# Kernel tuning notes

Measured on AMD Instinct MI355X. Metric: run time of the kernel, lower is better.

## Reference

```python
import jax, jax.numpy as jnp
import numpy as np

D = 2048          # input_dim == dec_hidden_size
S = 16384         # src_time_steps
H = 250           # projection hidden (hard-coded in module)


def setup_inputs() -> dict:
    key = jax.random.key(0)
    ks = jax.random.split(key, 12)
    sc_d = 1.0 / np.sqrt(D)
    sc_3d = 1.0 / np.sqrt(3 * D)
    sc_h = 1.0 / np.sqrt(H)
    return {
        "s_prev": jax.random.normal(ks[0], (1, 1, D), jnp.float32),
        "enc_hs": jax.random.normal(ks[1], (1, S, D), jnp.float32),
        "cur_men_rep": jax.random.normal(ks[2], (1, 1, D), jnp.float32),
        "src_mask": jax.random.randint(ks[3], (1, S), 0, 2, jnp.int32),
        "W_info": jax.random.normal(ks[4], (D, D), jnp.float32) * sc_d,
        "W_ctx": jax.random.normal(ks[5], (D, D), jnp.float32) * sc_d,
        "W_q": jax.random.normal(ks[6], (D, D), jnp.float32) * sc_d,
        "b_q": jnp.zeros((D,), jnp.float32),
        "W_p1": jax.random.normal(ks[7], (H, 3 * D), jnp.float32) * sc_3d,
        "b_p1": jnp.zeros((H,), jnp.float32),
        "W_p2": jax.random.normal(ks[8], (1, H), jnp.float32) * sc_h,
        "b_p2": jnp.zeros((1,), jnp.float32),
    }


def reference(s_prev, enc_hs, cur_men_rep, src_mask,
              W_info, W_ctx, W_q, b_q, W_p1, b_p1, W_p2, b_p2):
    # dh = linear_info(cur_men_rep): [1,1,D]; uh = linear_ctx(enc_hs): [1,S,D]
    dh = jnp.einsum('bqe,de->bqd', cur_men_rep, W_info)
    uh = jnp.einsum('bse,de->bsd', enc_hs, W_ctx)
    wq = jnp.einsum('bqe,de->bqd', s_prev, W_q) + b_q
    # cat(uh, wq.repeat, dh.repeat) -> tanh : [1,S,3D]
    wquh = jnp.tanh(jnp.concatenate(
        [uh, jnp.broadcast_to(wq, uh.shape), jnp.broadcast_to(dh, uh.shape)],
        axis=2))
    # projection: Linear(3D,250) -> Dropout(eval: identity) -> ReLU -> Linear(250,1)
    h = jax.nn.relu(jnp.einsum('bsk,hk->bsh', wquh, W_p1) + b_p1)
    scores = (jnp.einsum('bsh,oh->bso', h, W_p2) + b_p2).squeeze()   # [S] (B=1)
    scores = jnp.where(src_mask.squeeze().astype(bool), -jnp.inf, scores)
    attn = jax.nn.softmax(scores, axis=-1)                            # [S]
    ctx = jnp.sum(enc_hs * attn[None, :, None], axis=1)               # [1,D]
    return attn, ctx
```

## Files before the change

### kernel.cpp

```cpp
#include <hip/hip_runtime.h>
#include <hip/hip_bf16.h>
#include <stdint.h>

#define DD 2048
#define SS 16384
#define HH 250
#define GEMMB_GRID 264

typedef __attribute__((ext_vector_type(8))) short bf16x8;
typedef __attribute__((ext_vector_type(4))) float f32x4;

__device__ __forceinline__ unsigned short f2bf(float f){
  union { float f; uint32_t u; } v; v.f = f;
  uint32_t u = v.u;
  return (unsigned short)((u + 0x7fffu + ((u >> 16) & 1u)) >> 16);
}
__device__ __forceinline__ float fast_tanh(float x){
  return 1.0f - 2.0f / (1.0f + __expf(2.0f * x));
}
__device__ __forceinline__ void gl_lds16(const void* g, void* l){
  __builtin_amdgcn_global_load_lds((const __attribute__((address_space(1))) void*)g,
                                   (__attribute__((address_space(3))) void*)l, 16, 0, 0);
}

__global__ __launch_bounds__(256) void mega_kernel(
    const float* __restrict__ W_ctx, unsigned short* __restrict__ wctxb,
    const float* __restrict__ W_p1, unsigned short* __restrict__ wp1ab,
    const float* __restrict__ s_prev, const float* __restrict__ cmr,
    const float* __restrict__ Wq, const float* __restrict__ bq,
    const float* __restrict__ Winfo,
    float* __restrict__ twq, float* __restrict__ tdh,
    const int* __restrict__ mask, int* __restrict__ idx, int* __restrict__ cpos,
    int* __restrict__ mcount)
{
  const int b = blockIdx.x, t = threadIdx.x;
  if(b < 512){
    for(int i = b * 256 + t; i < (DD * DD) / 8; i += 512 * 256){
      const float4* p = (const float4*)(W_ctx + (size_t)i * 8);
      float4 a = p[0], c = p[1];
      bf16x8 v;
      v[0]=(short)f2bf(a.x); v[1]=(short)f2bf(a.y); v[2]=(short)f2bf(a.z); v[3]=(short)f2bf(a.w);
      v[4]=(short)f2bf(c.x); v[5]=(short)f2bf(c.y); v[6]=(short)f2bf(c.z); v[7]=(short)f2bf(c.w);
      *(bf16x8*)(wctxb + (size_t)i * 8) = v;
    }
  } else if(b < 768){
    int g = (b - 512) * 256 + t;
    int row = g >> 8, col = (g & 255) * 8;
    int rc = row < HH ? row : HH - 1;
    const float* s = W_p1 + (size_t)rc * (3 * DD) + col;
    bf16x8 v;
    #pragma unroll
    for(int j = 0; j < 8; j++) v[j] = (row < HH) ? (short)f2bf(s[j]) : (short)0;
    *(bf16x8*)(wp1ab + (size_t)g * 8) = v;
  } else if(b < 1792){
    int vb = b - 768;
    int wid = t >> 6, lane = t & 63;
    bool isq = vb < 512;
    int r = (isq ? vb : vb - 512) * 4 + wid;
    const float* M = (isq ? Wq : Winfo) + (size_t)r * DD;
    const float* x = isq ? s_prev : cmr;
    float s = 0.f;
    for(int i = lane; i < DD; i += 64) s += M[i] * x[i];
    #pragma unroll
    for(int o = 32; o; o >>= 1) s += __shfl_xor(s, o);
    if(lane == 0){
      if(isq) twq[r] = fast_tanh(s + bq[r]);
      else    tdh[r] = fast_tanh(s);
    }
  } else {
    __shared__ int cnt[256];
    const int base = t * 64;
    int c = 0;
    for(int i = 0; i < 64; i++) c += (mask[base + i] == 0);
    cnt[t] = c;
    __syncthreads();
    for(int off = 1; off < 256; off <<= 1){
      int v = (t >= off) ? cnt[t - off] : 0;
      __syncthreads();
      cnt[t] += v;
      __syncthreads();
    }
    int p = cnt[t] - c;
    for(int i = 0; i < 64; i++){
      int fi = base + i;
      if(mask[fi] == 0){ idx[p] = fi; cpos[fi] = p; p++; }
      else cpos[fi] = -1;
    }
    if(t == 255){
      int tot = cnt[255];
      mcount[0] = tot;
      mcount[1] = (tot + 255) & ~255;
      mcount[2] = (tot + 63) & ~63;
    }
  }
}

__global__ __launch_bounds__(256) void conv_enc_kernel(
    const float* __restrict__ enc, const int* __restrict__ idx,
    const int* __restrict__ mcount, unsigned short* __restrict__ out,
    const float* __restrict__ wp1, const float* __restrict__ bp1,
    const float* __restrict__ twq, const float* __restrict__ tdh,
    float* __restrict__ bias2)
{
  const int b = blockIdx.x, t = threadIdx.x;
  if(b < 2048){
    const int mc0 = mcount[0], mc1 = mcount[1];
    #pragma unroll
    for(int r = 0; r < 8; r++){
      int j = b * 8 + r;
      if(j >= mc1) return;
      unsigned short* o = out + (size_t)j * DD + t * 8;
      if(j >= mc0){
        bf16x8 z;
        #pragma unroll
        for(int i = 0; i < 8; i++) z[i] = 0;
        *(bf16x8*)o = z;
      } else {
        const float4* p = (const float4*)(enc + (size_t)idx[j] * DD + t * 8);
        float4 a = p[0], c = p[1];
        bf16x8 v;
        v[0]=(short)f2bf(a.x); v[1]=(short)f2bf(a.y); v[2]=(short)f2bf(a.z); v[3]=(short)f2bf(a.w);
        v[4]=(short)f2bf(c.x); v[5]=(short)f2bf(c.y); v[6]=(short)f2bf(c.z); v[7]=(short)f2bf(c.w);
        *(bf16x8*)o = v;
      }
    }
  } else {
    int h = (b - 2048) * 4 + (t >> 6);
    int lane = t & 63;
    if(h >= HH){ if(lane == 0 && h < 256) bias2[h] = 0.f; return; }
    const float* r1 = wp1 + (size_t)h * (3 * DD) + DD;
    const float* r2 = wp1 + (size_t)h * (3 * DD) + 2 * DD;
    float s = 0.f;
    for(int i = lane; i < DD; i += 64) s += r1[i] * twq[i] + r2[i] * tdh[i];
    #pragma unroll
    for(int o = 32; o; o >>= 1) s += __shfl_xor(s, o);
    if(lane == 0) bias2[h] = s + bp1[h];
  }
}

__device__ __forceinline__ void stage_half(const unsigned short* __restrict__ g,
                                           int grow0, int kt, char* ldsbase,
                                           int wid, int lane)
{
  const int srow = lane >> 3;
  const int c = (lane & 7) ^ srow;
  #pragma unroll
  for(int i = 0; i < 2; i++){
    int r8 = (wid * 2 + i) * 8;
    gl_lds16(g + (size_t)(grow0 + r8 + srow) * DD + kt + c * 8,
             ldsbase + r8 * 128);
  }
}
#define RDF(base, lr, kc) (*(const bf16x8*)((base) + (lr) * 128 + (((kc) * 16) ^ (((lr) & 7) << 4))))

__global__ __launch_bounds__(512, 2) void gemmA_kernel(
    const unsigned short* __restrict__ A, const unsigned short* __restrict__ B,
    const int* __restrict__ mcount, unsigned short* __restrict__ Ct)
{
  __shared__ alignas(128) char lds[131072];
  const int tid = threadIdx.x, lane = tid & 63, wid = tid >> 6;
  const int wm = wid >> 2, wn = wid & 3;
  const int slot = blockIdx.x >> 3;
  const int mt = (blockIdx.x & 7) + ((slot >> 3) << 3);
  const int n0 = (slot & 7) * 256;
  const int MT = mcount[1] >> 8;
  if(mt >= MT) return;
  const int m0 = mt * 256;
  const int frow = lane & 15, kch = lane >> 4;

  f32x4 acc[8][4] = {};

  stage_half(A, m0,        0, lds,                 wid, lane);
  stage_half(A, m0 + 128,  0, lds + 16384,         wid, lane);
  stage_half(B, n0,        0, lds + 32768,         wid, lane);
  stage_half(B, n0 + 128,  0, lds + 49152,         wid, lane);
  stage_half(B, n0,       64, lds + 65536 + 32768, wid, lane);
  stage_half(B, n0 + 128, 64, lds + 65536 + 49152, wid, lane);
  asm volatile("s_waitcnt vmcnt(4)" ::: "memory");
  __builtin_amdgcn_s_barrier();

  #pragma unroll 2
  for(int t = 0; t < 32; t++){
    const int d = t & 1;
    char* Ab = lds + d * 65536;
    char* Bb = Ab + 32768;
    char* An = lds + (d ^ 1) * 65536;
    bf16x8 bfr[4][2];
    #pragma unroll
    for(int q = 0; q < 4; q++){
      if(q == 0){
        #pragma unroll
        for(int nr = 0; nr < 4; nr++){
          int row = wn * 64 + nr * 16 + frow;
          #pragma unroll
          for(int ks = 0; ks < 2; ks++) bfr[nr][ks] = RDF(Bb, row, ks * 4 + kch);
        }
      }
      bf16x8 afr[2][2];
      #pragma unroll
      for(int mi = 0; mi < 2; mi++){
        int row = wm * 128 + (q * 2 + mi) * 16 + frow;
        #pragma unroll
        for(int ks = 0; ks < 2; ks++) afr[mi][ks] = RDF(Ab, row, ks * 4 + kch);
      }
      if(q == 0){
        if(t + 1 < 32){
          stage_half(A, m0,       (t + 1) * 64, An,         wid, lane);
          stage_half(A, m0 + 128, (t + 1) * 64, An + 16384, wid, lane);
        }
      } else if(q == 1){
        if(t + 2 < 32) stage_half(B, n0,       (t + 2) * 64, Bb,         wid, lane);
      } else if(q == 2){
        if(t + 2 < 32) stage_half(B, n0 + 128, (t + 2) * 64, Bb + 16384, wid, lane);
      }
      __builtin_amdgcn_s_barrier();
      __builtin_amdgcn_sched_barrier(0);
      __builtin_amdgcn_s_setprio(1);
      #pragma unroll
      for(int mi = 0; mi < 2; mi++)
        #pragma unroll
        for(int nr = 0; nr < 4; nr++)
          #pragma unroll
          for(int ks = 0; ks < 2; ks++)
            acc[q * 2 + mi][nr] = __builtin_amdgcn_mfma_f32_16x16x32_bf16(
                afr[mi][ks], bfr[nr][ks], acc[q * 2 + mi][nr], 0, 0, 0);
      __builtin_amdgcn_s_setprio(0);
      __builtin_amdgcn_sched_barrier(0);
      if(q == 3){
        if(t < 30)       asm volatile("s_waitcnt vmcnt(4)" ::: "memory");
        else if(t == 30) asm volatile("s_waitcnt vmcnt(0)" ::: "memory");
      }
      __builtin_amdgcn_s_barrier();
    }
  }

  const int r0 = m0 + wm * 128 + (lane >> 4) * 4;
  const int c0 = n0 + wn * 64 + frow;
  #pragma unroll
  for(int mr = 0; mr < 8; mr++)
    #pragma unroll
    for(int nr = 0; nr < 4; nr++)
      #pragma unroll
      for(int r = 0; r < 4; r++)
        Ct[(size_t)(r0 + mr * 16 + r) * DD + c0 + nr * 16] = f2bf(fast_tanh(acc[mr][nr][r]));
}

__global__ __launch_bounds__(512, 4) void gemmB_kernel(
    const unsigned short* __restrict__ A, const unsigned short* __restrict__ B,
    const int* __restrict__ mcount, const float* __restrict__ bias2,
    const float* __restrict__ w2, const float* __restrict__ bp2,
    float* __restrict__ attnc, float* __restrict__ Tpart)
{
  __shared__ alignas(128) char lds[81920];
  __shared__ float sred[8][32];
  const int tid = threadIdx.x, lane = tid & 63, wid = tid >> 6;
  const int wm = wid >> 2, wn = wid & 3;
  const int m0 = blockIdx.x * 64;
  const int mc0 = mcount[0], mc2 = mcount[2];
  if(m0 >= mc2){ if(tid == 0) Tpart[blockIdx.x] = 0.f; return; }
  const int frow = lane & 15, kch = lane >> 4;
  const int srow = lane >> 3, sc = ((lane & 7) ^ srow) * 8;

  f32x4 acc[2][4] = {};

  gl_lds16(A + (size_t)(m0 + wid * 8 + srow) * DD + sc, lds + wid * 1024);
  #pragma unroll
  for(int i = 0; i < 4; i++){
    int l = wid + 8 * i;
    gl_lds16(B + (size_t)(l * 8 + srow) * DD + sc,      lds + 16384 + l * 1024);
    gl_lds16(B + (size_t)(l * 8 + srow) * DD + 64 + sc, lds + 49152 + l * 1024);
  }
  asm volatile("s_waitcnt vmcnt(4)" ::: "memory");
  __builtin_amdgcn_s_barrier();

  #pragma unroll 2
  for(int t = 0; t < 32; t++){
    const int d = t & 1;
    char* Ab = lds + d * 8192;
    char* An = lds + (d ^ 1) * 8192;
    char* Bb = lds + 16384 + d * 32768;
    bf16x8 bfr[4][2], afr[2];
    #pragma unroll
    for(int q = 0; q < 2; q++){
      if(q == 0){
        #pragma unroll
        for(int nr = 0; nr < 4; nr++){
          int row = wn * 64 + nr * 16 + frow;
          #pragma unroll
          for(int ks = 0; ks < 2; ks++) bfr[nr][ks] = RDF(Bb, row, ks * 4 + kch);
        }
      }
      {
        int row = wm * 32 + q * 16 + frow;
        #pragma unroll
        for(int ks = 0; ks < 2; ks++) afr[ks] = RDF(Ab, row, ks * 4 + kch);
      }
      if(q == 0){
        if(t + 1 < 32)
          gl_lds16(A + (size_t)(m0 + wid * 8 + srow) * DD + (t + 1) * 64 + sc, An + wid * 1024);
      } else {
        if(t + 2 < 32){
          #pragma unroll
          for(int i = 0; i < 4; i++){
            int l = wid + 8 * i;
            gl_lds16(B + (size_t)(l * 8 + srow) * DD + (t + 2) * 64 + sc, Bb + l * 1024);
          }
        }
      }
      __builtin_amdgcn_s_barrier();
      __builtin_amdgcn_sched_barrier(0);
      __builtin_amdgcn_s_setprio(1);
      #pragma unroll
      for(int nr = 0; nr < 4; nr++)
        #pragma unroll
        for(int ks = 0; ks < 2; ks++)
          acc[q][nr] = __builtin_amdgcn_mfma_f32_16x16x32_bf16(afr[ks], bfr[nr][ks], acc[q][nr], 0, 0, 0);
      __builtin_amdgcn_s_setprio(0);
      __builtin_amdgcn_sched_barrier(0);
      if(q == 1){
        if(t < 30)       asm volatile("s_waitcnt vmcnt(4)" ::: "memory");
        else if(t == 30) asm volatile("s_waitcnt vmcnt(0)" ::: "memory");
      }
      __builtin_amdgcn_s_barrier();
    }
  }

  float w2v[4], b2v[4];
  #pragma unroll
  for(int in = 0; in < 4; in++){
    int n = wn * 64 + in * 16 + frow;
    w2v[in] = (n < HH) ? w2[n] : 0.f;
    b2v[in] = bias2[n];
  }
  #pragma unroll
  for(int mi = 0; mi < 2; mi++){
    #pragma unroll
    for(int r = 0; r < 4; r++){
      float s = 0.f;
      #pragma unroll
      for(int in = 0; in < 4; in++){
        float h = acc[mi][in][r] + b2v[in];
        s += (h > 0.f ? h : 0.f) * w2v[in];
      }
      s += __shfl_xor(s, 1); s += __shfl_xor(s, 2);
      s += __shfl_xor(s, 4); s += __shfl_xor(s, 8);
      if(frow == 0) sred[wid][mi * 16 + (lane >> 4) * 4 + r] = s;
    }
  }
  __syncthreads();
  if(tid < 64){
    int wmr = tid >> 5, rr = tid & 31;
    float s = sred[wmr * 4][rr] + sred[wmr * 4 + 1][rr] + sred[wmr * 4 + 2][rr]
            + sred[wmr * 4 + 3][rr] + bp2[0];
    int j = m0 + tid;
    float e = (j < mc0) ? __expf(s) : 0.f;
    if(j < mc0) attnc[j] = e;
    #pragma unroll
    for(int o = 32; o; o >>= 1) e += __shfl_xor(e, o);
    if(tid == 0) Tpart[blockIdx.x] = e;
  }
}

__global__ __launch_bounds__(256) void norm_kernel(
    const float* __restrict__ attnc, const int* __restrict__ cpos,
    const float* __restrict__ Tpart, float* __restrict__ out)
{
  __shared__ float sT;
  if(threadIdx.x == 0){
    float s = 0.f;
    for(int i = 0; i < GEMMB_GRID; i++) s += Tpart[i];
    sT = 1.0f / s;
  }
  __syncthreads();
  int i = blockIdx.x * 256 + threadIdx.x;
  int cp = cpos[i];
  out[i] = (cp >= 0) ? attnc[cp] * sT : 0.f;
}

__device__ __forceinline__ float bf2f(unsigned short h){
  union { uint32_t u; float f; } v; v.u = ((uint32_t)h) << 16; return v.f;
}
__global__ __launch_bounds__(256) void ctxp_kernel(
    const float* __restrict__ attnc, const unsigned short* __restrict__ encb,
    const int* __restrict__ mcount, float* __restrict__ part)
{
  const int b = blockIdx.x, t = threadIdx.x;
  const int mc0 = mcount[0];
  const int chunk = (mc0 + 255) >> 8;
  const int j0 = b * chunk;
  const int j1 = min(j0 + chunk, mc0);
  float a[8] = {};
  for(int j = j0; j < j1; j++){
    float e = attnc[j];
    bf16x8 v = *(const bf16x8*)(encb + (size_t)j * DD + t * 8);
    #pragma unroll
    for(int k = 0; k < 8; k++) a[k] += e * bf2f((unsigned short)v[k]);
  }
  float* o = part + (size_t)b * DD + t * 8;
  #pragma unroll
  for(int k = 0; k < 8; k++) o[k] = a[k];
}

__global__ __launch_bounds__(256) void ctxr_kernel(
    const float* __restrict__ part, const float* __restrict__ Tpart,
    float* __restrict__ out)
{
  __shared__ float sT;
  if(threadIdx.x == 0){
    float s = 0.f;
    for(int i = 0; i < GEMMB_GRID; i++) s += Tpart[i];
    sT = 1.0f / s;
  }
  __syncthreads();
  const int dcol = blockIdx.x * 256 + threadIdx.x;
  float s = 0.f;
  for(int b = 0; b < 256; b++) s += part[(size_t)b * DD + dcol];
  out[dcol] = s * sT;
}

extern "C" void kernel_launch(void* const* d_in, const int* in_sizes, int n_in,
                              void* d_out, int out_size, void* d_ws, size_t ws_size,
                              hipStream_t stream)
{
  const float* s_prev = (const float*)d_in[0];
  const float* enc    = (const float*)d_in[1];
  const float* cmr    = (const float*)d_in[2];
  const int*   mask   = (const int*)d_in[3];
  const float* W_info = (const float*)d_in[4];
  const float* W_ctx  = (const float*)d_in[5];
  const float* W_q    = (const float*)d_in[6];
  const float* b_q    = (const float*)d_in[7];
  const float* W_p1   = (const float*)d_in[8];
  const float* b_p1   = (const float*)d_in[9];
  const float* W_p2   = (const float*)d_in[10];
  const float* b_p2   = (const float*)d_in[11];
  float* out = (float*)d_out;

  char* ws = (char*)d_ws;
  unsigned short* encb    = (unsigned short*)(ws);
  unsigned short* tanhbuf = (unsigned short*)(ws + 67108864);
  unsigned short* wctxb   = (unsigned short*)(ws + 134217728);
  unsigned short* wp1ab   = (unsigned short*)(ws + 142606336);
  int*   idx    = (int*)(ws + 143654912);
  int*   cpos   = (int*)(ws + 143720448);
  float* attnc  = (float*)(ws + 143785984);
  float* part   = (float*)(ws + 143851520);
  float* twq    = (float*)(ws + 145948672);
  float* tdh    = (float*)(ws + 145956864);
  float* bias2  = (float*)(ws + 145965056);
  int*   mcount = (int*)(ws + 145966080);
  float* Tpart  = (float*)(ws + 145966208);

  mega_kernel<<<1793, 256, 0, stream>>>(W_ctx, wctxb, W_p1, wp1ab,
                                        s_prev, cmr, W_q, b_q, W_info,
                                        twq, tdh, mask, idx, cpos, mcount);
  conv_enc_kernel<<<2112, 256, 0, stream>>>(enc, idx, mcount, encb,
                                            W_p1, b_p1, twq, tdh, bias2);
  gemmA_kernel<<<512, 512, 0, stream>>>(encb, wctxb, mcount, tanhbuf);
  gemmB_kernel<<<GEMMB_GRID, 512, 0, stream>>>(tanhbuf, wp1ab, mcount, bias2,
                                               W_p2, b_p2, attnc, Tpart);
  norm_kernel<<<64, 256, 0, stream>>>(attnc, cpos, Tpart, out);
  ctxp_kernel<<<256, 256, 0, stream>>>(attnc, encb, mcount, part);
  ctxr_kernel<<<8, 256, 0, stream>>>(part, Tpart, out + SS);
}
```

Measured before the change: 194.3 us.

## Coalesce weight conversions, ballot-based mask compaction, fuse norm and ctx partial kernels

The W_ctx and W_p1 bf16 conversion branches now use per-thread float4-to-bf16x4 accesses that coalesce across threads, and fewer blocks each do more work. Mask compaction becomes a wave-ballot prefix scan over interleaved elements, so reads are coalesced. This replaces the strided per-thread serial loop and the LDS scan. The norm and ctx-partial kernels merge into one launch to save a kernel dispatch. The ballot scan adds two block barriers per iteration across 64 iterations, which could lengthen the single compaction block.

```diff
diff --git a/kernel.cpp b/kernel.cpp
--- a/kernel.cpp
+++ b/kernel.cpp
@@ -8,12 +8,21 @@
 #define GEMMB_GRID 264
 
 typedef __attribute__((ext_vector_type(8))) short bf16x8;
+typedef __attribute__((ext_vector_type(4))) short bf16x4;
 typedef __attribute__((ext_vector_type(4))) float f32x4;
 
 __device__ __forceinline__ unsigned short f2bf(float f){
   union { float f; uint32_t u; } v; v.f = f;
   uint32_t u = v.u;
   return (unsigned short)((u + 0x7fffu + ((u >> 16) & 1u)) >> 16);
+}
+__device__ __forceinline__ float bf2f(unsigned short h){
+  union { uint32_t u; float f; } v; v.u = ((uint32_t)h) << 16; return v.f;
+}
+__device__ __forceinline__ bf16x4 pk4(float4 a){
+  bf16x4 v;
+  v[0]=(short)f2bf(a.x); v[1]=(short)f2bf(a.y); v[2]=(short)f2bf(a.z); v[3]=(short)f2bf(a.w);
+  return v;
 }
 __device__ __forceinline__ float fast_tanh(float x){
   return 1.0f - 2.0f / (1.0f + __expf(2.0f * x));
@@ -34,26 +43,28 @@
     int* __restrict__ mcount)
 {
   const int b = blockIdx.x, t = threadIdx.x;
-  if(b < 512){
-    for(int i = b * 256 + t; i < (DD * DD) / 8; i += 512 * 256){
-      const float4* p = (const float4*)(W_ctx + (size_t)i * 8);
-      float4 a = p[0], c = p[1];
-      bf16x8 v;
-      v[0]=(short)f2bf(a.x); v[1]=(short)f2bf(a.y); v[2]=(short)f2bf(a.z); v[3]=(short)f2bf(a.w);
-      v[4]=(short)f2bf(c.x); v[5]=(short)f2bf(c.y); v[6]=(short)f2bf(c.z); v[7]=(short)f2bf(c.w);
-      *(bf16x8*)(wctxb + (size_t)i * 8) = v;
-    }
-  } else if(b < 768){
-    int g = (b - 512) * 256 + t;
-    int row = g >> 8, col = (g & 255) * 8;
-    int rc = row < HH ? row : HH - 1;
-    const float* s = W_p1 + (size_t)rc * (3 * DD) + col;
-    bf16x8 v;
-    #pragma unroll
-    for(int j = 0; j < 8; j++) v[j] = (row < HH) ? (short)f2bf(s[j]) : (short)0;
-    *(bf16x8*)(wp1ab + (size_t)g * 8) = v;
-  } else if(b < 1792){
-    int vb = b - 768;
+  if(b < 256){
+    const float4* in4 = (const float4*)W_ctx;
+    bf16x4* out4 = (bf16x4*)wctxb;
+    const int gt = b * 256 + t;
+    for(int i = gt; i < 1048576; i += 65536) out4[i] = pk4(in4[i]);
+  } else if(b < 288){
+    bf16x4* out4 = (bf16x4*)wp1ab;
+    const int gt = (b - 256) * 256 + t;
+    #pragma unroll
+    for(int k = 0; k < 16; k++){
+      int i = gt + k * 8192;
+      int row = i >> 9, col = i & 511;
+      bf16x4 v;
+      if(row < HH){
+        v = pk4(*(const float4*)(W_p1 + (size_t)row * (3 * DD) + (col << 2)));
+      } else {
+        v[0] = 0; v[1] = 0; v[2] = 0; v[3] = 0;
+      }
+      out4[i] = v;
+    }
+  } else if(b < 1312){
+    int vb = b - 288;
     int wid = t >> 6, lane = t & 63;
     bool isq = vb < 512;
     int r = (isq ? vb : vb - 512) * 4 + wid;
@@ -68,29 +79,29 @@
       else    tdh[r] = fast_tanh(s);
     }
   } else {
-    __shared__ int cnt[256];
-    const int base = t * 64;
-    int c = 0;
-    for(int i = 0; i < 64; i++) c += (mask[base + i] == 0);
-    cnt[t] = c;
-    __syncthreads();
-    for(int off = 1; off < 256; off <<= 1){
-      int v = (t >= off) ? cnt[t - off] : 0;
+    __shared__ int wsum[4];
+    const int lane = t & 63, w = t >> 6;
+    int running = 0;
+    for(int k = 0; k < 64; k++){
+      const int e = k * 256 + t;
+      const int m = (mask[e] == 0);
+      unsigned long long bal = __ballot(m);
+      if(lane == 0) wsum[w] = __popcll(bal);
       __syncthreads();
-      cnt[t] += v;
+      int wpre = 0;
+      #pragma unroll
+      for(int i = 0; i < 4; i++) if(i < w) wpre += wsum[i];
+      int tot = wsum[0] + wsum[1] + wsum[2] + wsum[3];
+      const int lpre = __popcll(bal & ((1ull << lane) - 1ull));
+      const int pos = running + wpre + lpre;
+      if(m){ idx[pos] = e; cpos[e] = pos; } else cpos[e] = -1;
+      running += tot;
       __syncthreads();
     }
-    int p = cnt[t] - c;
-    for(int i = 0; i < 64; i++){
-      int fi = base + i;
-      if(mask[fi] == 0){ idx[p] = fi; cpos[fi] = p; p++; }
-      else cpos[fi] = -1;
-    }
-    if(t == 255){
-      int tot = cnt[255];
-      mcount[0] = tot;
-      mcount[1] = (tot + 255) & ~255;
-      mcount[2] = (tot + 63) & ~63;
+    if(t == 0){
+      mcount[0] = running;
+      mcount[1] = (running + 255) & ~255;
+      mcount[2] = (running + 63) & ~63;
     }
   }
 }
@@ -361,44 +372,41 @@
   }
 }
 
-__global__ __launch_bounds__(256) void norm_kernel(
+__global__ __launch_bounds__(256) void normctx_kernel(
     const float* __restrict__ attnc, const int* __restrict__ cpos,
-    const float* __restrict__ Tpart, float* __restrict__ out)
-{
-  __shared__ float sT;
-  if(threadIdx.x == 0){
-    float s = 0.f;
-    for(int i = 0; i < GEMMB_GRID; i++) s += Tpart[i];
-    sT = 1.0f / s;
-  }
-  __syncthreads();
-  int i = blockIdx.x * 256 + threadIdx.x;
-  int cp = cpos[i];
-  out[i] = (cp >= 0) ? attnc[cp] * sT : 0.f;
-}
-
-__device__ __forceinline__ float bf2f(unsigned short h){
-  union { uint32_t u; float f; } v; v.u = ((uint32_t)h) << 16; return v.f;
-}
-__global__ __launch_bounds__(256) void ctxp_kernel(
-    const float* __restrict__ attnc, const unsigned short* __restrict__ encb,
-    const int* __restrict__ mcount, float* __restrict__ part)
+    const int* __restrict__ mcount, const float* __restrict__ Tpart,
+    const unsigned short* __restrict__ encb,
+    float* __restrict__ out, float* __restrict__ part)
 {
   const int b = blockIdx.x, t = threadIdx.x;
-  const int mc0 = mcount[0];
-  const int chunk = (mc0 + 255) >> 8;
-  const int j0 = b * chunk;
-  const int j1 = min(j0 + chunk, mc0);
-  float a[8] = {};
-  for(int j = j0; j < j1; j++){
-    float e = attnc[j];
-    bf16x8 v = *(const bf16x8*)(encb + (size_t)j * DD + t * 8);
-    #pragma unroll
-    for(int k = 0; k < 8; k++) a[k] += e * bf2f((unsigned short)v[k]);
-  }
-  float* o = part + (size_t)b * DD + t * 8;
-  #pragma unroll
-  for(int k = 0; k < 8; k++) o[k] = a[k];
+  if(b < 64){
+    __shared__ float sT;
+    if(t == 0){
+      float s = 0.f;
+      for(int i = 0; i < GEMMB_GRID; i++) s += Tpart[i];
+      sT = 1.0f / s;
+    }
+    __syncthreads();
+    int i = b * 256 + t;
+    int cp = cpos[i];
+    out[i] = (cp >= 0) ? attnc[cp] * sT : 0.f;
+  } else {
+    const int bb = b - 64;
+    const int mc0 = mcount[0];
+    const int chunk = (mc0 + 255) >> 8;
+    const int j0 = bb * chunk;
+    const int j1 = min(j0 + chunk, mc0);
+    float a[8] = {};
+    for(int j = j0; j < j1; j++){
+      float e = attnc[j];
+      bf16x8 v = *(const bf16x8*)(encb + (size_t)j * DD + t * 8);
+      #pragma unroll
+      for(int k = 0; k < 8; k++) a[k] += e * bf2f((unsigned short)v[k]);
+    }
+    float* o = part + (size_t)bb * DD + t * 8;
+    #pragma unroll
+    for(int k = 0; k < 8; k++) o[k] = a[k];
+  }
 }
 
 __global__ __launch_bounds__(256) void ctxr_kernel(
@@ -451,7 +459,7 @@
   int*   mcount = (int*)(ws + 145966080);
   float* Tpart  = (float*)(ws + 145966208);
 
-  mega_kernel<<<1793, 256, 0, stream>>>(W_ctx, wctxb, W_p1, wp1ab,
+  mega_kernel<<<1313, 256, 0, stream>>>(W_ctx, wctxb, W_p1, wp1ab,
                                         s_prev, cmr, W_q, b_q, W_info,
                                         twq, tdh, mask, idx, cpos, mcount);
   conv_enc_kernel<<<2112, 256, 0, stream>>>(enc, idx, mcount, encb,
@@ -459,7 +467,7 @@
   gemmA_kernel<<<512, 512, 0, stream>>>(encb, wctxb, mcount, tanhbuf);
   gemmB_kernel<<<GEMMB_GRID, 512, 0, stream>>>(tanhbuf, wp1ab, mcount, bias2,
                                                W_p2, b_p2, attnc, Tpart);
-  norm_kernel<<<64, 256, 0, stream>>>(attnc, cpos, Tpart, out);
-  ctxp_kernel<<<256, 256, 0, stream>>>(attnc, encb, mcount, part);
+  normctx_kernel<<<320, 256, 0, stream>>>(attnc, cpos, mcount, Tpart,
+                                          encb, out, part);
   ctxr_kernel<<<8, 256, 0, stream>>>(part, Tpart, out + SS);
 }
```

Measured after the change: 178.8 us. 8.0% less time.
